# Optimization experiments

Hardware: AMD Instinct MI355X
Metric: run time of the kernel (lower is better)

## Reference

```python
import jax, jax.numpy as jnp
import numpy as np
import itertools

DIM, ORDER = 8, 4  # matches init_kwargs

def _exponent_table(dim, order):
    # All multisets (non-decreasing tuples) of size 0..order over range(dim),
    # sorted lexicographically -- identical to sorted(Counter keys) in the torch code
    # (Counter keys are sorted tuples; combinations_with_replacement yields exactly those).
    terms = sorted(itertools.chain.from_iterable(
        itertools.combinations_with_replacement(range(dim), o) for o in range(order + 1)))
    E = np.zeros((len(terms), dim), dtype=np.int32)
    for i, t in enumerate(terms):
        for d in t:
            E[i, d] += 1
    return E

E = jnp.asarray(_exponent_table(DIM, ORDER))  # [nterms=495, dim=8]


def setup_inputs() -> dict:
    key = jax.random.key(0)
    x = jax.random.normal(key, (65536, DIM), dtype=jnp.float32)
    return {"x": x}


def reference(x):
    # torch: cat_i prod_d x[..., d] ** ind_i.count(d)
    # vectorized: broadcast pow with exponent table, reduce-product over dim axis
    # x: [B, dim] -> [B, 1, dim] ** [nterms, dim] -> prod over dim -> [B, nterms]
    return jnp.prod(x[..., None, :] ** E, axis=-1)
```

## Files before the change

### kernel.cpp

```cpp
#include <hip/hip_runtime.h>


struct Specs {
    unsigned short uv[8][64];
    unsigned short pp[64];
};

constexpr int pidx_c(int a, int b) {
    return 9 + 8 * a - (a * (a - 1)) / 2 + (b - a);
}

constexpr Specs make_specs() {
    Specs S{};
    for (int l = 0; l < 64; ++l) {
        int s1 = 0, s2 = 0, u1 = 0, u2 = 0;
        if (l >= 1 && l <= 8) { s1 = l - 1; u1 = 1; }
        else if (l >= 9 && l < 45) {
            int k = l - 9, i = 0;
            while (k >= 8 - i) { k -= 8 - i; ++i; }
            s1 = i; s2 = i + k; u1 = 1; u2 = 1;
        }
        S.pp[l] = (unsigned short)(s1 | (s2 << 4) | (u1 << 8) | (u2 << 9));
    }
    int idx = 1;
    for (int a = 0; a < 8; ++a) {
        S.uv[idx >> 6][idx & 63] = (unsigned short)(1 + a); ++idx;
        for (int b = a; b < 8; ++b) {
            S.uv[idx >> 6][idx & 63] = (unsigned short)pidx_c(a, b); ++idx;
            for (int c = b; c < 8; ++c) {
                S.uv[idx >> 6][idx & 63] =
                    (unsigned short)(pidx_c(a, b) | ((1 + c) << 8)); ++idx;
                for (int d = c; d < 8; ++d) {
                    S.uv[idx >> 6][idx & 63] =
                        (unsigned short)(pidx_c(a, b) | (pidx_c(c, d) << 8));
                    ++idx;
                }
            }
        }
    }
    return S;
}

__constant__ Specs SPECS = make_specs();

__global__ __launch_bounds__(64) void TotalDegree_29755533426739_kernel(
    const float* __restrict__ x, float* __restrict__ out, int B, int rows_per_wave) {
    const int lane = (int)threadIdx.x;

    const int ppv  = SPECS.pp[lane];
    const int s1   = ppv & 15;
    const int s2   = (ppv >> 4) & 15;
    const bool use1 = ((ppv >> 8) & 1) != 0;
    const bool use2 = ((ppv >> 9) & 1) != 0;

    int uspec[8], vspec[8];
    #pragma unroll
    for (int c = 0; c < 8; ++c) {
        const int sp = (int)SPECS.uv[c][lane];
        uspec[c] = sp & 255;
        vspec[c] = sp >> 8;
    }

    int row0 = (int)blockIdx.x * rows_per_wave;
    int row1 = row0 + rows_per_wave;
    if (row1 > B) row1 = B;

    for (int row = row0; row < row1; ++row) {
        const float* x8 = x + (size_t)row * 8;
        const float a1 = x8[s1];
        const float a2 = x8[s2];
        const float P  = (use1 ? a1 : 1.0f) * (use2 ? a2 : 1.0f);

        float* orow = out + (size_t)row * 495;
        #pragma unroll
        for (int c = 0; c < 8; ++c) {
            const float f1 = __shfl(P, uspec[c], 64);
            const float f2 = __shfl(P, vspec[c], 64);
            const float tv = f1 * f2;
            const int t = c * 64 + lane;
            if (t < 495) orow[t] = tv;
        }
    }
}

extern "C" void kernel_launch(void* const* d_in, const int* in_sizes, int n_in,
                              void* d_out, int out_size, void* d_ws, size_t ws_size,
                              hipStream_t stream) {
    const float* x = (const float*)d_in[0];
    float* out = (float*)d_out;
    const int B = in_sizes[0] / 8;
    const int ROWS = 16;
    const int grid = (B + ROWS - 1) / ROWS;
    hipLaunchKernelGGL(TotalDegree_29755533426739_kernel,
                       dim3(grid), dim3(64), 0, stream, x, out, B, ROWS);
}
```

Measured before the change: 137.1 us.

## Stage input rows in shared memory with 4-wave blocks and transposed spec table

Moves from one-wave blocks that each handle 16 rows to 256-thread blocks. Each block cooperatively loads 32 rows of x into LDS with a single coalesced load, then each wave computes 8 rows. The spec table is transposed so every lane reads its 8 contiguous entries, and the inner row loop is partially unrolled. The aim is to replace scattered per-row global loads with LDS reads and to raise occupancy, at the cost of a barrier and LDS use per block.

After: 131.6 us. 1.04x faster.

```diff
diff --git a/kernel.cpp b/kernel.cpp
--- a/kernel.cpp
+++ b/kernel.cpp
@@ -2,7 +2,7 @@
 
 
 struct Specs {
-    unsigned short uv[8][64];
+    unsigned short uv[64][8];
     unsigned short pp[64];
 };
 
@@ -24,14 +24,14 @@
     }
     int idx = 1;
     for (int a = 0; a < 8; ++a) {
-        S.uv[idx >> 6][idx & 63] = (unsigned short)(1 + a); ++idx;
+        S.uv[idx & 63][idx >> 6] = (unsigned short)(1 + a); ++idx;
         for (int b = a; b < 8; ++b) {
-            S.uv[idx >> 6][idx & 63] = (unsigned short)pidx_c(a, b); ++idx;
+            S.uv[idx & 63][idx >> 6] = (unsigned short)pidx_c(a, b); ++idx;
             for (int c = b; c < 8; ++c) {
-                S.uv[idx >> 6][idx & 63] =
+                S.uv[idx & 63][idx >> 6] =
                     (unsigned short)(pidx_c(a, b) | ((1 + c) << 8)); ++idx;
                 for (int d = c; d < 8; ++d) {
-                    S.uv[idx >> 6][idx & 63] =
+                    S.uv[idx & 63][idx >> 6] =
                         (unsigned short)(pidx_c(a, b) | (pidx_c(c, d) << 8));
                     ++idx;
                 }
@@ -43,11 +43,23 @@
 
 __constant__ Specs SPECS = make_specs();
 
-__global__ __launch_bounds__(64) void TotalDegree_29755533426739_kernel(
-    const float* __restrict__ x, float* __restrict__ out, int B, int rows_per_wave) {
-    const int lane = (int)threadIdx.x;
+#define ROWS_PER_BLOCK 32
+#define ROWS_PER_WAVE  8
 
-    const int ppv  = SPECS.pp[lane];
+__global__ __launch_bounds__(256, 4) void TotalDegree_29755533426739_kernel(
+    const float* __restrict__ x, float* __restrict__ out, int B) {
+    __shared__ float xs[ROWS_PER_BLOCK * 8];
+
+    const int tid  = (int)threadIdx.x;
+    const int lane = tid & 63;
+    const int wid  = tid >> 6;
+
+    {
+        const int gi = (int)blockIdx.x * (ROWS_PER_BLOCK * 8) + tid;
+        xs[tid] = (gi < B * 8) ? x[gi] : 0.0f;
+    }
+
+    const int ppv  = (int)SPECS.pp[lane];
     const int s1   = ppv & 15;
     const int s2   = (ppv >> 4) & 15;
     const bool use1 = ((ppv >> 8) & 1) != 0;
@@ -56,29 +68,30 @@
     int uspec[8], vspec[8];
     #pragma unroll
     for (int c = 0; c < 8; ++c) {
-        const int sp = (int)SPECS.uv[c][lane];
+        const int sp = (int)SPECS.uv[lane][c];
         uspec[c] = sp & 255;
         vspec[c] = sp >> 8;
     }
 
-    int row0 = (int)blockIdx.x * rows_per_wave;
-    int row1 = row0 + rows_per_wave;
-    if (row1 > B) row1 = B;
+    __syncthreads();
 
-    for (int row = row0; row < row1; ++row) {
-        const float* x8 = x + (size_t)row * 8;
-        const float a1 = x8[s1];
-        const float a2 = x8[s2];
-        const float P  = (use1 ? a1 : 1.0f) * (use2 ? a2 : 1.0f);
+    #pragma unroll 2
+    for (int rr = 0; rr < ROWS_PER_WAVE; ++rr) {
+        const int r    = wid * ROWS_PER_WAVE + rr;
+        const int grow = (int)blockIdx.x * ROWS_PER_BLOCK + r;
+        if (grow < B) {
+            const float a1 = xs[r * 8 + s1];
+            const float a2 = xs[r * 8 + s2];
+            const float P  = (use1 ? a1 : 1.0f) * (use2 ? a2 : 1.0f);
 
-        float* orow = out + (size_t)row * 495;
-        #pragma unroll
-        for (int c = 0; c < 8; ++c) {
-            const float f1 = __shfl(P, uspec[c], 64);
-            const float f2 = __shfl(P, vspec[c], 64);
-            const float tv = f1 * f2;
-            const int t = c * 64 + lane;
-            if (t < 495) orow[t] = tv;
+            float* orow = out + (size_t)grow * 495;
+            #pragma unroll
+            for (int c = 0; c < 8; ++c) {
+                const float f1 = __shfl(P, uspec[c], 64);
+                const float f2 = __shfl(P, vspec[c], 64);
+                const int t = c * 64 + lane;
+                if (t < 495) orow[t] = f1 * f2;
+            }
         }
     }
 }
@@ -89,8 +102,7 @@
     const float* x = (const float*)d_in[0];
     float* out = (float*)d_out;
     const int B = in_sizes[0] / 8;
-    const int ROWS = 16;
-    const int grid = (B + ROWS - 1) / ROWS;
+    const int grid = (B + ROWS_PER_BLOCK - 1) / ROWS_PER_BLOCK;
     hipLaunchKernelGGL(TotalDegree_29755533426739_kernel,
-                       dim3(grid), dim3(64), 0, stream, x, out, B, ROWS);
+                       dim3(grid), dim3(256), 0, stream, x, out, B);
 }
```
